# Kernel tuning notes

Hardware: AMD Instinct MI355X
Metric: run time of the kernel (lower is better)

The kernel has to match this reference:

```python
import jax, jax.numpy as jnp
import numpy as np

B, T, L, H = 16, 16, 512, 768


def setup_inputs() -> dict:
    key = jax.random.key(0)
    k1, k2, k3, k4, k5, k6 = jax.random.split(key, 6)
    hn = jax.random.normal(k1, (B, L, H), dtype=jnp.float32)
    decoder_out = jax.random.normal(k2, (B, L, H), dtype=jnp.float32)
    W1 = jax.random.normal(k3, (H, H), dtype=jnp.float32) * (1.0 / np.sqrt(H))
    W2 = jax.random.normal(k4, (H, H), dtype=jnp.float32) * (1.0 / np.sqrt(H))
    V = jax.random.normal(k5, (H,), dtype=jnp.float32) * (1.0 / np.sqrt(H))
    # Ragged, consistent pointer indices: T monotone segment starts per sample,
    # gold boundary Yindex[b,t] in [Xindex[b,t], L).
    step = L // T  # 32
    Xindex = jnp.broadcast_to(jnp.arange(T, dtype=jnp.int64) * step, (B, T))
    offsets = jax.random.randint(k6, (B, T), 0, step, dtype=jnp.int64)
    Yindex = Xindex + offsets
    lens = jnp.full((B,), L, dtype=jnp.int64)
    return {"hn": hn, "decoder_out": decoder_out, "W1": W1, "W2": W2, "V": V,
            "Xindex": Xindex, "Yindex": Yindex, "lens": lens}


def reference(hn, decoder_out, W1, W2, V, Xindex, Yindex, lens):
    # Faithful batched form of training_decoder + pointerLayer:
    #   for each sample i, step j:
    #     en = hn[i, Xindex[i,j]:lens[i]]            (ragged suffix)
    #     dj = decoder_out[i, Yindex[i,j]]           (cur_dj = decoder_out[cur_groundy])
    #     s  = selu(V @ selu(W1 en + W2 dj))
    #     loss += NLL(log_softmax(s), Yindex[i,j]-Xindex[i,j])
    WE = jnp.einsum('blh,gh->blg', hn, W1)                        # [B,L,H]  nnW1(en)
    dj = jnp.take_along_axis(decoder_out, Yindex[:, :, None], axis=1)  # [B,T,H]
    WD = jnp.einsum('bth,gh->btg', dj, W2)                        # [B,T,H]  nnW2(dj)
    act = jax.nn.selu(WE[:, None, :, :] + WD[:, :, None, :])      # [B,T,L,H]
    scores = jax.nn.selu(jnp.einsum('btlh,h->btl', act, V))       # [B,T,L]
    pos = jnp.arange(hn.shape[1])
    mask = (pos[None, None, :] >= Xindex[:, :, None]) & (pos[None, None, :] < lens[:, None, None])
    neg_inf = jnp.finfo(scores.dtype).min
    masked = jnp.where(mask, scores, neg_inf)
    logp = masked - jax.scipy.special.logsumexp(masked, axis=-1, keepdims=True)
    # logits index (Yindex - Xindex) in the sliced array == global index Yindex
    gold = jnp.take_along_axis(logp, Yindex[:, :, None], axis=-1)[..., 0]  # [B,T]
    return -jnp.mean(gold)
```

## Files before the change

### kernel.cpp

```cpp
#include <hip/hip_runtime.h>
#include <hip/hip_bf16.h>
#include <math.h>

#define SELU_SCALE 1.0507009873554805f
#define SELU_ALPHA 1.6732632423543772f

static constexpr int B_ = 16, T_ = 16, L_ = 512, H_ = 768;
static constexpr int WSZ = 768 * 768;
static constexpr int HNELEM = B_ * L_ * H_;
static constexpr int DJELEM = B_ * T_ * H_;
static constexpr int ALLELEM = HNELEM + 2 * WSZ + DJELEM;

typedef __bf16 bf16x8 __attribute__((ext_vector_type(8)));
typedef float  f32x4  __attribute__((ext_vector_type(4)));

__device__ __forceinline__ float bf_lo(unsigned u) { return __uint_as_float(u << 16); }
__device__ __forceinline__ float bf_hi(unsigned u) { return __uint_as_float(u & 0xFFFF0000u); }

__device__ __forceinline__ float selu_core(float x) {
    float e = fmaf(__expf(x), SELU_ALPHA, -SELU_ALPHA);
    return x > 0.0f ? x : e;
}

__device__ __forceinline__ int xsw(int r) { return (r >> 1) & 3; }

__device__ __forceinline__ bf16x8 pack8(float4 a, float4 b) {
    bf16x8 o;
    o[0] = (__bf16)a.x; o[1] = (__bf16)a.y; o[2] = (__bf16)a.z; o[3] = (__bf16)a.w;
    o[4] = (__bf16)b.x; o[5] = (__bf16)b.y; o[6] = (__bf16)b.z; o[7] = (__bf16)b.w;
    return o;
}

__global__ __launch_bounds__(256) void prep_k(
        const float* __restrict__ hn, const float* __restrict__ dec,
        const float* __restrict__ w1, const float* __restrict__ w2,
        const int* __restrict__ Yi,
        __bf16* __restrict__ allb, float* __restrict__ out) {
    if (blockIdx.x == 0 && threadIdx.x == 0) out[0] = 0.0f;
    int idx = (blockIdx.x * 256 + threadIdx.x) * 8;
    const float* src;
    if (idx < HNELEM) {
        src = hn + idx;
    } else if (idx < HNELEM + WSZ) {
        src = w1 + (idx - HNELEM);
    } else if (idx < HNELEM + 2 * WSZ) {
        src = w2 + (idx - HNELEM - WSZ);
    } else {
        int e = idx - (HNELEM + 2 * WSZ);
        int r = e / 768, c = e - r * 768;
        src = dec + ((size_t)((r >> 4) * L_ + Yi[r])) * H_ + c;
    }
    float4 a = *(const float4*)src;
    float4 b = *(const float4*)(src + 4);
    *(bf16x8*)(allb + idx) = pack8(a, b);
}

__global__ __launch_bounds__(256, 2) void gemm_k(
        const __bf16* __restrict__ allb,
        __bf16* __restrict__ web, float* __restrict__ wdf) {
    __shared__ __bf16 sm[2][2][4096];

    int bx = blockIdx.x;
    const __bf16 *Ab, *Bb; int m0, n0; bool wd;
    if (bx < 384) {
        wd = false; Ab = allb; Bb = allb + HNELEM;
        m0 = (bx & 63) * 128; n0 = (bx >> 6) * 128;
    } else {
        wd = true; bx -= 384;
        Ab = allb + HNELEM + 2 * WSZ; Bb = allb + HNELEM + WSZ;
        m0 = (bx & 1) * 128;  n0 = (bx >> 1) * 128;
    }

    const int tid = threadIdx.x, wave = tid >> 6, lane = tid & 63;
    const int wm = (wave >> 1) * 64, wn = (wave & 1) * 64;
    const int lr = lane & 15, q = lane >> 4;
    const int l4 = lane >> 2, sl = lane & 3;

    const int ar0 = wave * 16 + l4, ar1 = ar0 + 64;
    const __bf16* gA0 = Ab + (size_t)(m0 + ar0) * 768 + (sl ^ xsw(ar0)) * 8;
    const __bf16* gA1 = Ab + (size_t)(m0 + ar1) * 768 + (sl ^ xsw(ar1)) * 8;
    const __bf16* gB0 = Bb + (size_t)(n0 + ar0) * 768 + (sl ^ xsw(ar0)) * 8;
    const __bf16* gB1 = Bb + (size_t)(n0 + ar1) * 768 + (sl ^ xsw(ar1)) * 8;
    const int ld0 = wave * 512;
    const int ld1 = 2048 + wave * 512;

    const int aoff0 = (wm + lr) * 32 + (q ^ xsw(wm + lr)) * 8;
    const int boff0 = (wn + lr) * 32 + (q ^ xsw(wn + lr)) * 8;

    f32x4 acc[4][4] = {};

#define STAGE(b, kk)                                                                        \
    {                                                                                       \
        __builtin_amdgcn_global_load_lds((const __attribute__((address_space(1))) void*)(gA0 + (kk)), \
            (__attribute__((address_space(3))) void*)&sm[b][0][ld0], 16, 0, 0);             \
        __builtin_amdgcn_global_load_lds((const __attribute__((address_space(1))) void*)(gA1 + (kk)), \
            (__attribute__((address_space(3))) void*)&sm[b][0][ld1], 16, 0, 0);             \
        __builtin_amdgcn_global_load_lds((const __attribute__((address_space(1))) void*)(gB0 + (kk)), \
            (__attribute__((address_space(3))) void*)&sm[b][1][ld0], 16, 0, 0);             \
        __builtin_amdgcn_global_load_lds((const __attribute__((address_space(1))) void*)(gB1 + (kk)), \
            (__attribute__((address_space(3))) void*)&sm[b][1][ld1], 16, 0, 0);             \
    }

#define COMPUTE(b)                                                                          \
    {                                                                                       \
        bf16x8 af[4], bfr[4];                                                               \
        _Pragma("unroll")                                                                   \
        for (int i = 0; i < 4; ++i) af[i]  = *(const bf16x8*)&sm[b][0][aoff0 + i * 512];    \
        _Pragma("unroll")                                                                   \
        for (int j = 0; j < 4; ++j) bfr[j] = *(const bf16x8*)&sm[b][1][boff0 + j * 512];    \
        _Pragma("unroll")                                                                   \
        for (int i = 0; i < 4; ++i)                                                         \
            _Pragma("unroll")                                                               \
            for (int j = 0; j < 4; ++j)                                                     \
                acc[i][j] = __builtin_amdgcn_mfma_f32_16x16x32_bf16(af[i], bfr[j], acc[i][j], 0, 0, 0); \
    }

    STAGE(0, 0)
    asm volatile("s_waitcnt vmcnt(0)" ::: "memory");
    __builtin_amdgcn_s_barrier();

    int cur = 0;
#pragma unroll 1
    for (int t = 0; t < 23; ++t) {
        STAGE(cur ^ 1, (t + 1) * 32)
        COMPUTE(cur)
        asm volatile("s_waitcnt vmcnt(0)" ::: "memory");
        __builtin_amdgcn_s_barrier();
        cur ^= 1;
    }
    COMPUTE(cur)
#undef STAGE
#undef COMPUTE

#pragma unroll
    for (int i = 0; i < 4; ++i)
#pragma unroll
        for (int j = 0; j < 4; ++j)
#pragma unroll
            for (int r = 0; r < 4; ++r) {
                int row = m0 + wm + i * 16 + q * 4 + r;
                int col = n0 + wn + j * 16 + lr;
                if (!wd) web[(size_t)row * 768 + col] = (__bf16)acc[i][j][r];
                else     wdf[(size_t)row * 768 + col] = acc[i][j][r];
            }
}

__global__ __launch_bounds__(256, 4) void scores_k(
        const __bf16* __restrict__ web, const float* __restrict__ wdf,
        const float* __restrict__ V, const int* __restrict__ Xi,
        float* __restrict__ scores) {
    const int b  = blockIdx.x;
    const int l0 = ((int)gridDim.y - 1 - (int)blockIdx.y) * 16;
    const int t0 = blockIdx.z * 8;
    const int tid = threadIdx.x;
    const int ls = tid >> 4, hc = tid & 15;
    const int l  = l0 + ls;
    const int h0 = hc * 8;

    float we[48], vv[48];
    const __bf16* wr = web + ((size_t)(b * L_ + l)) * H_ + h0;
#pragma unroll
    for (int j = 0; j < 6; ++j) {
        uint4 u = *(const uint4*)(wr + j * 128);
        we[j*8+0] = bf_lo(u.x); we[j*8+1] = bf_hi(u.x);
        we[j*8+2] = bf_lo(u.y); we[j*8+3] = bf_hi(u.y);
        we[j*8+4] = bf_lo(u.z); we[j*8+5] = bf_hi(u.z);
        we[j*8+6] = bf_lo(u.w); we[j*8+7] = bf_hi(u.w);
    }
    const float* vp = V + h0;
#pragma unroll
    for (int j = 0; j < 6; ++j) {
        float4 a = *(const float4*)(vp + j * 128);
        float4 c = *(const float4*)(vp + j * 128 + 4);
        vv[j*8+0] = a.x; vv[j*8+1] = a.y; vv[j*8+2] = a.z; vv[j*8+3] = a.w;
        vv[j*8+4] = c.x; vv[j*8+5] = c.y; vv[j*8+6] = c.z; vv[j*8+7] = c.w;
    }

    const int wmaxl = l0 + ((tid >> 6) << 2) + 3;
    const int bT = b * T_;
#pragma unroll 1
    for (int t = t0; t < t0 + 8; ++t) {
        const int X = Xi[bT + t];
        if (wmaxl < X) continue;
        const float* wdp = wdf + ((size_t)(bT + t)) * H_ + h0;
        float a0 = 0.f, a1 = 0.f, a2 = 0.f, a3 = 0.f;
#pragma unroll
        for (int j = 0; j < 6; ++j) {
            float4 x = *(const float4*)(wdp + j * 128);
            float4 y = *(const float4*)(wdp + j * 128 + 4);
            a0 = fmaf(selu_core(we[j*8+0] + x.x), vv[j*8+0], a0);
            a1 = fmaf(selu_core(we[j*8+1] + x.y), vv[j*8+1], a1);
            a2 = fmaf(selu_core(we[j*8+2] + x.z), vv[j*8+2], a2);
            a3 = fmaf(selu_core(we[j*8+3] + x.w), vv[j*8+3], a3);
            a0 = fmaf(selu_core(we[j*8+4] + y.x), vv[j*8+4], a0);
            a1 = fmaf(selu_core(we[j*8+5] + y.y), vv[j*8+5], a1);
            a2 = fmaf(selu_core(we[j*8+6] + y.z), vv[j*8+6], a2);
            a3 = fmaf(selu_core(we[j*8+7] + y.w), vv[j*8+7], a3);
        }
        float dot = (a0 + a1) + (a2 + a3);
        dot += __shfl_xor(dot, 1);
        dot += __shfl_xor(dot, 2);
        dot += __shfl_xor(dot, 4);
        dot += __shfl_xor(dot, 8);
        if (hc == 0) {
            dot *= SELU_SCALE;
            float sc = dot > 0.0f ? SELU_SCALE * dot
                                  : SELU_SCALE * SELU_ALPHA * (__expf(dot) - 1.0f);
            scores[((size_t)(bT + t)) * L_ + l] = sc;
        }
    }
}

__global__ __launch_bounds__(64) void loss_k(
        const float* __restrict__ scores, const int* __restrict__ Xi,
        const int* __restrict__ Yi, float* __restrict__ out) {
    const int bt = blockIdx.x;
    const int lane = threadIdx.x;
    const int X = Xi[bt];
    const int Y = Yi[bt];
    const float* row = scores + (size_t)bt * L_;

    float m = -INFINITY;
    for (int l = X + lane; l < L_; l += 64) m = fmaxf(m, row[l]);
#pragma unroll
    for (int off = 32; off > 0; off >>= 1) m = fmaxf(m, __shfl_xor(m, off));

    float s = 0.0f;
    for (int l = X + lane; l < L_; l += 64) s += __expf(row[l] - m);
#pragma unroll
    for (int off = 32; off > 0; off >>= 1) s += __shfl_xor(s, off);

    if (lane == 0)
        atomicAdd(out, (m + __logf(s) - row[Y]) * (1.0f / (B_ * T_)));
}

extern "C" void kernel_launch(void* const* d_in, const int* in_sizes, int n_in,
                              void* d_out, int out_size, void* d_ws, size_t ws_size,
                              hipStream_t stream) {
    const float* hn  = (const float*)d_in[0];
    const float* dec = (const float*)d_in[1];
    const float* W1  = (const float*)d_in[2];
    const float* W2  = (const float*)d_in[3];
    const float* V   = (const float*)d_in[4];
    const int*   Xi  = (const int*)d_in[5];
    const int*   Yi  = (const int*)d_in[6];
    float* out = (float*)d_out;

    char* ws = (char*)d_ws;
    size_t off = 0;
    auto alloc = [&](size_t bytes) -> char* {
        char* p = ws + off;
        off += (bytes + 255) & ~(size_t)255;
        return p;
    };
    __bf16* web    = (__bf16*)alloc((size_t)B_ * L_ * H_ * 2);
    float*  wdf    = (float*)alloc((size_t)B_ * T_ * H_ * 4);
    float*  scores = (float*)alloc((size_t)B_ * T_ * L_ * 4);
    __bf16* allb   = (__bf16*)alloc((size_t)ALLELEM * 2);

    prep_k<<<ALLELEM / (256 * 8), 256, 0, stream>>>(hn, dec, W1, W2, Yi, allb, out);
    gemm_k<<<396, 256, 0, stream>>>(allb, web, wdf);
    scores_k<<<dim3(B_, L_ / 16, 2), 256, 0, stream>>>(web, wdf, V, Xi, scores);
    loss_k<<<B_ * T_, 64, 0, stream>>>(scores, Xi, Yi, out);
}
```

Measured before the change: 148.9 us.

## Triple-buffer GEMM LDS pipeline and early-exit masked scores waves

The GEMM main loop moves from double to triple buffering in LDS. Loads are issued two K-tiles ahead and each step waits only on the older loads (vmcnt(4)) rather than draining all of them, so global loads overlap more with MFMA work. The scores kernel now computes the last valid t up front and returns early for waves whose rows are all masked, which skips the WE/V register loads there, and its t-loop is unrolled by 2. The cost is more LDS per block, which may reduce occupancy, plus extra register pressure from the unroll.

```diff
diff --git a/kernel.cpp b/kernel.cpp
--- a/kernel.cpp
+++ b/kernel.cpp
@@ -58,7 +58,7 @@
 __global__ __launch_bounds__(256, 2) void gemm_k(
         const __bf16* __restrict__ allb,
         __bf16* __restrict__ web, float* __restrict__ wdf) {
-    __shared__ __bf16 sm[2][2][4096];
+    __shared__ __bf16 sm[3][2][4096];
 
     int bx = blockIdx.x;
     const __bf16 *Ab, *Bb; int m0, n0; bool wd;
@@ -115,20 +115,32 @@
                 acc[i][j] = __builtin_amdgcn_mfma_f32_16x16x32_bf16(af[i], bfr[j], acc[i][j], 0, 0, 0); \
     }
 
+#define ITER(tt, bc, bs)                                                                    \
+    {                                                                                       \
+        asm volatile("s_waitcnt vmcnt(4)" ::: "memory");                                    \
+        __builtin_amdgcn_s_barrier();                                                       \
+        __builtin_amdgcn_sched_barrier(0);                                                  \
+        if ((tt) + 2 < 24) STAGE(bs, ((tt) + 2) * 32)                                       \
+        COMPUTE(bc)                                                                         \
+    }
+
     STAGE(0, 0)
+    STAGE(1, 32)
+
+#pragma unroll 1
+    for (int g = 0; g < 7; ++g) {
+        const int t0g = g * 3;
+        ITER(t0g + 0, 0, 2)
+        ITER(t0g + 1, 1, 0)
+        ITER(t0g + 2, 2, 1)
+    }
+    ITER(21, 0, 2)
+    ITER(22, 1, 0)
     asm volatile("s_waitcnt vmcnt(0)" ::: "memory");
     __builtin_amdgcn_s_barrier();
-
-    int cur = 0;
-#pragma unroll 1
-    for (int t = 0; t < 23; ++t) {
-        STAGE(cur ^ 1, (t + 1) * 32)
-        COMPUTE(cur)
-        asm volatile("s_waitcnt vmcnt(0)" ::: "memory");
-        __builtin_amdgcn_s_barrier();
-        cur ^= 1;
-    }
-    COMPUTE(cur)
+    __builtin_amdgcn_sched_barrier(0);
+    COMPUTE(2)
+#undef ITER
 #undef STAGE
 #undef COMPUTE
 
@@ -156,6 +168,14 @@
     const int ls = tid >> 4, hc = tid & 15;
     const int l  = l0 + ls;
     const int h0 = hc * 8;
+    const int bT = b * T_;
+
+    const int wmaxl = l0 + ((tid >> 6) << 2) + 3;
+    if (wmaxl < Xi[bT + t0]) return;
+    int tend = t0;
+#pragma unroll
+    for (int tt = t0; tt < t0 + 8; ++tt)
+        if (wmaxl >= Xi[bT + tt]) tend = tt + 1;
 
     float we[48], vv[48];
     const __bf16* wr = web + ((size_t)(b * L_ + l)) * H_ + h0;
@@ -176,12 +196,8 @@
         vv[j*8+4] = c.x; vv[j*8+5] = c.y; vv[j*8+6] = c.z; vv[j*8+7] = c.w;
     }
 
-    const int wmaxl = l0 + ((tid >> 6) << 2) + 3;
-    const int bT = b * T_;
-#pragma unroll 1
-    for (int t = t0; t < t0 + 8; ++t) {
-        const int X = Xi[bT + t];
-        if (wmaxl < X) continue;
+#pragma unroll 2
+    for (int t = t0; t < tend; ++t) {
         const float* wdp = wdf + ((size_t)(bT + t)) * H_ + h0;
         float a0 = 0.f, a1 = 0.f, a2 = 0.f, a3 = 0.f;
 #pragma unroll
```

Result: faster. 145.1 us (-2.5%).
